# Performance work log

Hardware: AMD Instinct MI355X
Metric: run time of the kernel (lower is better)

Reference implementation:

```python
import jax, jax.numpy as jnp
import numpy as np

B, L, W, C = 16, 200, 64, 128
H_INTRA = 64   # intra_hidden // 2 per direction
H_INTER = 128
EPS = 1e-8


def layer_norm(x, gamma, beta):
    mu = jnp.mean(x, axis=-1, keepdims=True)
    var = jnp.mean(jnp.square(x - mu), axis=-1, keepdims=True)
    return (x - mu) * jax.lax.rsqrt(var + EPS) * gamma + beta


def gru_seq(x, Wk, Uk, b, H):
    """Keras GRU, reset_after=False, recurrent_activation=sigmoid. x: [N,T,D] -> [N,T,H]."""
    xw = jnp.einsum('ntd,dk->ntk', x, Wk) + b  # precompute input projections [N,T,3H]
    def step(h, xw_t):
        z = jax.nn.sigmoid(xw_t[:, :H] + h @ Uk[:, :H])
        r = jax.nn.sigmoid(xw_t[:, H:2 * H] + h @ Uk[:, H:2 * H])
        hh = jnp.tanh(xw_t[:, 2 * H:] + (r * h) @ Uk[:, 2 * H:])
        h = z * h + (1.0 - z) * hh
        return h, h
    h0 = jnp.zeros((x.shape[0], H), x.dtype)
    _, ys = jax.lax.scan(step, h0, jnp.swapaxes(xw, 0, 1))  # [T,N,H]
    return jnp.swapaxes(ys, 0, 1)


def skip_gru_seq(x, Wk, Uk, b, Wp, bp, H):
    """Skip-RNN GRU (Campos et al.): binary update gate u_t conditionally updates state.
    Returns (outputs [N,T,H], gates [N,T,1])."""
    xw = jnp.einsum('ntd,dk->ntk', x, Wk) + b
    def step(carry, xw_t):
        h, ut = carry
        # straight-through binarization of cumulative update prob
        u = ut + jax.lax.stop_gradient(jnp.round(ut) - ut)  # [N,1]
        z = jax.nn.sigmoid(xw_t[:, :H] + h @ Uk[:, :H])
        r = jax.nn.sigmoid(xw_t[:, H:2 * H] + h @ Uk[:, H:2 * H])
        hh = jnp.tanh(xw_t[:, 2 * H:] + (r * h) @ Uk[:, 2 * H:])
        h_new = z * h + (1.0 - z) * hh
        h = u * h_new + (1.0 - u) * h  # skip: copy state when u == 0
        delta = jax.nn.sigmoid(h @ Wp + bp)  # [N,1]
        ut_next = u * delta + (1.0 - u) * (ut + jnp.minimum(delta, 1.0 - ut))
        return (h, ut_next), (h, u)
    N = x.shape[0]
    h0 = jnp.zeros((N, H), x.dtype)
    ut0 = jnp.ones((N, 1), x.dtype)
    _, (ys, us) = jax.lax.scan(step, (h0, ut0), jnp.swapaxes(xw, 0, 1))
    return jnp.swapaxes(ys, 0, 1), jnp.swapaxes(us, 0, 1)


def setup_inputs():
    key = jax.random.key(0)
    ks = jax.random.split(key, 16)
    rn = lambda k, s: jax.random.normal(k, s, dtype=jnp.float32) * 0.05
    z = lambda s: jnp.zeros(s, jnp.float32)
    o = lambda s: jnp.ones(s, jnp.float32)
    return {
        'x': jax.random.normal(ks[0], (B, L, W, C), dtype=jnp.float32),
        'scale': jax.random.uniform(ks[1], (B, L, W, 1), dtype=jnp.float32),
        'Wf': rn(ks[2], (C, 3 * H_INTRA)), 'Uf': rn(ks[3], (H_INTRA, 3 * H_INTRA)), 'bf': z((3 * H_INTRA,)),
        'Wb': rn(ks[4], (C, 3 * H_INTRA)), 'Ub': rn(ks[5], (H_INTRA, 3 * H_INTRA)), 'bb': z((3 * H_INTRA,)),
        'W_intra_fc': rn(ks[6], (2 * H_INTRA, C)), 'b_intra_fc': z((C,)),
        'g_intra': o((C,)), 'beta_intra': z((C,)),
        'Wi': rn(ks[7], (C + 1, 3 * H_INTER)), 'Ui': rn(ks[8], (H_INTER, 3 * H_INTER)), 'bi': z((3 * H_INTER,)),
        'Wp': rn(ks[9], (H_INTER, 1)), 'bp': z((1,)),
        'W_inter_fc': rn(ks[10], (H_INTER, C)), 'b_inter_fc': z((C,)),
        'g_inter': o((C,)), 'beta_inter': z((C,)),
    }


def reference(x, scale, Wf, Uf, bf, Wb, Ub, bb, W_intra_fc, b_intra_fc, g_intra, beta_intra,
              Wi, Ui, bi, Wp, bp, W_inter_fc, b_inter_fc, g_inter, beta_inter):
    # ----- intra path: bidirectional GRU over the width axis -----
    intra_in = x.reshape(B * L, W, C)
    out_f = gru_seq(intra_in, Wf, Uf, bf, H_INTRA)
    out_b = gru_seq(intra_in[:, ::-1, :], Wb, Ub, bb, H_INTRA)[:, ::-1, :]
    intra_rnn_out = jnp.concatenate([out_f, out_b], axis=-1)  # [B*L, W, 2H]
    update_gate_intra = jnp.ones((64, L), jnp.float32)  # skip=0 branch: constant ones
    intra_dense = intra_rnn_out @ W_intra_fc + b_intra_fc  # [B*L, W, C]
    intra_out = x + layer_norm(intra_dense.reshape(B, L, W, C), g_intra, beta_intra)
    # ----- inter path: skip-GRU over the L (time) axis -----
    inter_in = jnp.transpose(intra_out, (0, 2, 1, 3)).reshape(B * W, L, C)
    scale2 = jnp.transpose(scale, (0, 2, 1, 3)).reshape(B * W, L, 1)
    inter_in = jnp.concatenate([inter_in, scale2], axis=-1)  # [B*W, L, C+1]
    inter_rnn_out, gates = skip_gru_seq(inter_in, Wi, Ui, bi, Wp, bp, H_INTER)
    update_gate_inter = gates[:, :, 0]  # [B*W, L]
    inter_dense = (inter_rnn_out @ W_inter_fc + b_inter_fc).reshape(B, W, L, C)
    inter_ln_in = jnp.transpose(inter_dense, (0, 2, 1, 3))  # [B, L, W, C]
    inter_out = intra_out + layer_norm(inter_ln_in, g_inter, beta_inter)
    return inter_out, update_gate_intra, update_gate_inter
```

## Files before the change

### kernel.cpp

```cpp
#include <hip/hip_runtime.h>
#include <cmath>


typedef float f32x16 __attribute__((ext_vector_type(16)));

__device__ __forceinline__ float sigf(float x) { return 1.0f / (1.0f + expf(-x)); }
__device__ __forceinline__ float rlanef(float v, int l) {
  return __uint_as_float(__builtin_amdgcn_readlane(__float_as_uint(v), (unsigned)l));
}
__device__ __forceinline__ void ldsbar() {
  asm volatile("s_waitcnt lgkmcnt(0)" ::: "memory");
  __builtin_amdgcn_s_barrier();
  __builtin_amdgcn_sched_barrier(0);
}

template <int SB>
__device__ __forceinline__ void macP2(const f32x16& u0, const f32x16& u1, float hv,
                                      float& a0, float& a1) {
#pragma unroll
  for (int k = 0; k < 16; ++k) {
    const float hs = rlanef(hv, SB + k);
    a0 = fmaf(u0[k], hs, a0);
    a1 = fmaf(u1[k], hs, a1);
  }
}
template <int SB>
__device__ __forceinline__ void macP1(const f32x16& u, float hv, float& a) {
#pragma unroll
  for (int k = 0; k < 16; ++k) a = fmaf(u[k], rlanef(hv, SB + k), a);
}

__global__ __launch_bounds__(256) void k_fill_ones(float* __restrict__ p, int n) {
  int i = blockIdx.x * 256 + threadIdx.x;
  if (i < n) p[i] = 1.0f;
}

enum { MA_X_FWD = 0, MA_X_BWD = 1, MA_INTER = 2 };

template <int MODE>
__global__ __launch_bounds__(256) void k_gemm_xw(
    const float* __restrict__ A0, const float* __restrict__ A1,
    const float* __restrict__ Bm, const float* __restrict__ bias,
    float* __restrict__ Cm, long M0, int N, int K, int KT)
{
  __shared__ float As[16][132];
  __shared__ float Bs[16][68];
  const int tid = threadIdx.x;
  const int tx = tid & 15, ty = tid >> 4;
  const long row0g = M0 + (long)blockIdx.x * 128;
  const int col0 = blockIdx.y * 64;
  const int lr = tid >> 1;
  const int lk8 = (tid & 1) * 8;
  const int bk = tid >> 4;
  const int bc4 = (tid & 15) * 4;
  float acc[8][4];
#pragma unroll
  for (int i = 0; i < 8; ++i)
#pragma unroll
    for (int j = 0; j < 4; ++j) acc[i][j] = 0.f;

  const long rg = row0g + lr;
  long abase = 0, rowc = 0;
  if (MODE == MA_X_FWD) {
    abase = rg * 128;
  } else if (MODE == MA_X_BWD) {
    const long s = rg >> 6; const int t = (int)(rg & 63);
    abase = (s * 64 + (63 - t)) * 128;
  } else {
    const int n = (int)(rg & 1023);
    const int l = (int)(rg >> 10);
    rowc = ((long)(n >> 6) * 200 + l) * 64 + (n & 63);
    abase = rowc * 128;
  }

  for (int kt = 0; kt < KT; ++kt) {
    const int k0 = kt * 16;
    {
      float v[8];
      if (MODE != MA_INTER || kt < 8) {
        const float4 a0 = *reinterpret_cast<const float4*>(&A0[abase + k0 + lk8]);
        const float4 a1 = *reinterpret_cast<const float4*>(&A0[abase + k0 + lk8 + 4]);
        v[0] = a0.x; v[1] = a0.y; v[2] = a0.z; v[3] = a0.w;
        v[4] = a1.x; v[5] = a1.y; v[6] = a1.z; v[7] = a1.w;
      } else {
#pragma unroll
        for (int j = 0; j < 8; ++j) {
          const int k = k0 + lk8 + j;
          v[j] = (k < 128) ? A0[abase + k] : ((k == 128) ? A1[rowc] : 0.f);
        }
      }
#pragma unroll
      for (int j = 0; j < 8; ++j) As[lk8 + j][lr] = v[j];
    }
    {
      const int k = k0 + bk;
      float4 b4 = make_float4(0.f, 0.f, 0.f, 0.f);
      if (k < K) b4 = *reinterpret_cast<const float4*>(&Bm[(long)k * N + col0 + bc4]);
      *reinterpret_cast<float4*>(&Bs[bk][bc4]) = b4;
    }
    __syncthreads();
#pragma unroll
    for (int kk = 0; kk < 16; ++kk) {
      const float4 a0 = *reinterpret_cast<const float4*>(&As[kk][ty * 8]);
      const float4 a1 = *reinterpret_cast<const float4*>(&As[kk][ty * 8 + 4]);
      const float4 b4 = *reinterpret_cast<const float4*>(&Bs[kk][tx * 4]);
      const float av[8] = {a0.x, a0.y, a0.z, a0.w, a1.x, a1.y, a1.z, a1.w};
      const float bv[4] = {b4.x, b4.y, b4.z, b4.w};
#pragma unroll
      for (int i = 0; i < 8; ++i)
#pragma unroll
        for (int j = 0; j < 4; ++j) acc[i][j] = fmaf(av[i], bv[j], acc[i][j]);
    }
    __syncthreads();
  }
  const float4 bi4 = *reinterpret_cast<const float4*>(&bias[col0 + tx * 4]);
#pragma unroll
  for (int i = 0; i < 8; ++i) {
    const long rl = (long)blockIdx.x * 128 + ty * 8 + i;
    float4 o;
    o.x = acc[i][0] + bi4.x;
    o.y = acc[i][1] + bi4.y;
    o.z = acc[i][2] + bi4.z;
    o.w = acc[i][3] + bi4.w;
    *reinterpret_cast<float4*>(&Cm[rl * (long)N + col0 + tx * 4]) = o;
  }
}

__global__ __attribute__((amdgpu_waves_per_eu(4, 4))) __launch_bounds__(256)
void k_gru_intra5(
    const float* __restrict__ xwf, const float* __restrict__ xwb,
    const float* __restrict__ Uf, const float* __restrict__ Ub,
    float* __restrict__ rnn)
{
  const int dir = blockIdx.y;
  const float* __restrict__ xw = dir ? xwb : xwf;
  const float* __restrict__ U  = dir ? Ub : Uf;
  __shared__ float h8[4][64], z8[4][64], rh8[4][64];
  __shared__ float pA[4][4][128];
  __shared__ float pB[4][4][64];
  const int tid = threadIdx.x;
  const int w = tid >> 6, lane = tid & 63;
  const long s0 = (long)blockIdx.x * 4;

  f32x16 uz, ur, uhh;
#pragma unroll
  for (int k = 0; k < 16; ++k) {
    const int row = (w * 16 + k) * 192;
    uz[k]  = U[row + lane];
    ur[k]  = U[row + 64 + lane];
    uhh[k] = U[row + 128 + lane];
  }
  h8[w][lane] = 0.f;
  __syncthreads();

  const long xrow0 = (s0 + w) * 64;
  float xa1 = xw[xrow0 * 192 + lane];
  float xa2 = xw[xrow0 * 192 + 64 + lane];
  float xb  = xw[xrow0 * 192 + 128 + lane];

  for (int t = 0; t < 64; ++t) {
    const int tn = (t < 63) ? t + 1 : t;
    const float xa1n = xw[(xrow0 + tn) * 192 + lane];
    const float xa2n = xw[(xrow0 + tn) * 192 + 64 + lane];
    const float xbn  = xw[(xrow0 + tn) * 192 + 128 + lane];
    {
      const float hv01 = h8[lane >> 5][w * 16 + (lane & 15)];
      const float hv23 = h8[2 + (lane >> 5)][w * 16 + (lane & 15)];
      float az0 = 0.f, ar0 = 0.f, az1 = 0.f, ar1 = 0.f;
      float az2 = 0.f, ar2 = 0.f, az3 = 0.f, ar3 = 0.f;
      macP2<0>(uz, ur, hv01, az0, ar0);
      macP2<32>(uz, ur, hv01, az1, ar1);
      macP2<0>(uz, ur, hv23, az2, ar2);
      macP2<32>(uz, ur, hv23, az3, ar3);
      pA[0][w][lane] = az0; pA[0][w][64 + lane] = ar0;
      pA[1][w][lane] = az1; pA[1][w][64 + lane] = ar1;
      pA[2][w][lane] = az2; pA[2][w][64 + lane] = ar2;
      pA[3][w][lane] = az3; pA[3][w][64 + lane] = ar3;
    }
    ldsbar();
    {
      const float sz = pA[w][0][lane] + pA[w][1][lane] + pA[w][2][lane] +
                       pA[w][3][lane] + xa1;
      const float sr = pA[w][0][64 + lane] + pA[w][1][64 + lane] +
                       pA[w][2][64 + lane] + pA[w][3][64 + lane] + xa2;
      z8[w][lane] = sigf(sz);
      rh8[w][lane] = sigf(sr) * h8[w][lane];
    }
    ldsbar();
    {
      const float rv01 = rh8[lane >> 5][w * 16 + (lane & 15)];
      const float rv23 = rh8[2 + (lane >> 5)][w * 16 + (lane & 15)];
      float a0 = 0.f, a1 = 0.f, a2 = 0.f, a3 = 0.f;
      macP1<0>(uhh, rv01, a0);
      macP1<32>(uhh, rv01, a1);
      macP1<0>(uhh, rv23, a2);
      macP1<32>(uhh, rv23, a3);
      pB[0][w][lane] = a0;
      pB[1][w][lane] = a1;
      pB[2][w][lane] = a2;
      pB[3][w][lane] = a3;
    }
    ldsbar();
    {
      const float pre = pB[w][0][lane] + pB[w][1][lane] + pB[w][2][lane] +
                        pB[w][3][lane] + xb;
      const float hh = tanhf(pre);
      const float z = z8[w][lane];
      const float ho = h8[w][lane];
      const float hn = z * ho + (1.f - z) * hh;
      h8[w][lane] = hn;
      const int tt = dir ? (63 - t) : t;
      rnn[((s0 + w) * 64 + tt) * 128 + dir * 64 + lane] = hn;
    }
    ldsbar();
    xa1 = xa1n; xa2 = xa2n; xb = xbn;
  }
}

__global__ __attribute__((amdgpu_waves_per_eu(4, 4))) __launch_bounds__(1024)
void k_gru_inter10(
    const float* __restrict__ xw, const float* __restrict__ Ui,
    const float* __restrict__ Wp, const float* __restrict__ bp,
    float* __restrict__ rnn, float* __restrict__ gates,
    float* __restrict__ hstate, float* __restrict__ ustate,
    int t0, int nt)
{
  __shared__ float h4[4][128], z4[4][128], rh4[4][128];
  __shared__ float pA[4][8][256];
  __shared__ float pB[4][8][128];
  __shared__ float uu[4], utt[4];
  const int tid = threadIdx.x;
  const int w = tid >> 6, lane = tid & 63;
  const int kq = w & 7;
  const int kb = kq << 4;
  const int cg = w >> 3;
  const int n0 = blockIdx.x * 4;

  f32x16 uz0, uz1, uh;
#pragma unroll
  for (int k = 0; k < 16; ++k) {
    const long r = (long)(kb + k) * 384;
    uz0[k] = Ui[r + cg * 128 + lane];
    uz1[k] = Ui[r + cg * 128 + 64 + lane];
    uh[k]  = Ui[r + 256 + cg * 64 + lane];
  }
  if (tid < 512) {
    const int s = tid >> 7, c = tid & 127;
    h4[s][c] = (t0 == 0) ? 0.f : hstate[(long)(n0 + s) * 128 + c];
  }
  if (tid < 4) {
    utt[tid] = (t0 == 0) ? 1.f : ustate[n0 + tid];
    uu[tid]  = (t0 == 0) ? 1.f : ustate[1024 + n0 + tid];
  }
  const float bp0 = bp[0];
  float wpA = 0.f, wpB = 0.f;
  if (w < 4) { wpA = Wp[lane]; wpB = Wp[64 + lane]; }
  __syncthreads();

  const int sC = tid >> 8;
  const int cC = tid & 255;
  float xc = xw[(long)(n0 + sC) * 384 + cC];
  float xbA = 0.f, xbB = 0.f;
  if (w < 4) {
    xbA = xw[(long)(n0 + w) * 384 + 256 + lane];
    xbB = xw[(long)(n0 + w) * 384 + 320 + lane];
  }

  for (int dl = 0; dl < nt; ++dl) {
    const float u0g = uu[0], u1g = uu[1], u2g = uu[2], u3g = uu[3];
    const bool act = (u0g + u1g + u2g + u3g) != 0.f;
    const int dn = (dl + 1 < nt) ? dl + 1 : dl;
    const float xcn = xw[((long)dn * 1024 + n0 + sC) * 384 + cC];
    float xbAn = 0.f, xbBn = 0.f;
    if (w < 4) {
      xbAn = xw[((long)dn * 1024 + n0 + w) * 384 + 256 + lane];
      xbBn = xw[((long)dn * 1024 + n0 + w) * 384 + 320 + lane];
    }
    if (act) {
      {
        const float hv01 = h4[lane >> 5][kb + (lane & 15)];
        const float hv23 = h4[2 + (lane >> 5)][kb + (lane & 15)];
        if (u0g != 0.f) {
          float a0 = 0.f, a1 = 0.f;
          macP2<0>(uz0, uz1, hv01, a0, a1);
          pA[0][kq][cg * 128 + lane] = a0;
          pA[0][kq][cg * 128 + 64 + lane] = a1;
        }
        if (u1g != 0.f) {
          float a0 = 0.f, a1 = 0.f;
          macP2<32>(uz0, uz1, hv01, a0, a1);
          pA[1][kq][cg * 128 + lane] = a0;
          pA[1][kq][cg * 128 + 64 + lane] = a1;
        }
        if (u2g != 0.f) {
          float a0 = 0.f, a1 = 0.f;
          macP2<0>(uz0, uz1, hv23, a0, a1);
          pA[2][kq][cg * 128 + lane] = a0;
          pA[2][kq][cg * 128 + 64 + lane] = a1;
        }
        if (u3g != 0.f) {
          float a0 = 0.f, a1 = 0.f;
          macP2<32>(uz0, uz1, hv23, a0, a1);
          pA[3][kq][cg * 128 + lane] = a0;
          pA[3][kq][cg * 128 + 64 + lane] = a1;
        }
      }
      ldsbar();
      {
        if (uu[sC] != 0.f) {
          float sum = xc;
#pragma unroll
          for (int q = 0; q < 8; ++q) sum += pA[sC][q][cC];
          if (cC < 128) z4[sC][cC] = sigf(sum);
          else rh4[sC][cC - 128] = sigf(sum) * h4[sC][cC - 128];
        }
      }
      ldsbar();
      {
        const float rv01 = rh4[lane >> 5][kb + (lane & 15)];
        const float rv23 = rh4[2 + (lane >> 5)][kb + (lane & 15)];
        const int cB = cg * 64 + lane;
        if (u0g != 0.f) {
          float b = 0.f;
          macP1<0>(uh, rv01, b);
          pB[0][kq][cB] = b;
        }
        if (u1g != 0.f) {
          float b = 0.f;
          macP1<32>(uh, rv01, b);
          pB[1][kq][cB] = b;
        }
        if (u2g != 0.f) {
          float b = 0.f;
          macP1<0>(uh, rv23, b);
          pB[2][kq][cB] = b;
        }
        if (u3g != 0.f) {
          float b = 0.f;
          macP1<32>(uh, rv23, b);
          pB[3][kq][cB] = b;
        }
      }
      ldsbar();
      if (w < 4) {
        const float us = uu[w];
        const float hoA = h4[w][lane], hoB = h4[w][64 + lane];
        float hqA, hqB;
        if (us != 0.f) {
          float sA = xbA, sB = xbB;
#pragma unroll
          for (int q = 0; q < 8; ++q) {
            sA += pB[w][q][lane];
            sB += pB[w][q][64 + lane];
          }
          const float hhA = tanhf(sA), hhB = tanhf(sB);
          const float zA = z4[w][lane], zB = z4[w][64 + lane];
          hqA = zA * hoA + (1.f - zA) * hhA;
          hqB = zB * hoB + (1.f - zB) * hhB;
          h4[w][lane] = hqA;
          h4[w][64 + lane] = hqB;
        } else {
          hqA = hoA; hqB = hoB;
        }
        rnn[((long)dl * 1024 + n0 + w) * 128 + lane] = hqA;
        rnn[((long)dl * 1024 + n0 + w) * 128 + 64 + lane] = hqB;
        float p = hqA * wpA + hqB * wpB;
        p += __shfl_xor(p, 32);
        p += __shfl_xor(p, 16);
        p += __shfl_xor(p, 8);
        p += __shfl_xor(p, 4);
        p += __shfl_xor(p, 2);
        p += __shfl_xor(p, 1);
        if (lane == 0) {
          const float delta = sigf(p + bp0);
          const float ut = utt[w];
          gates[(long)(n0 + w) * 200 + t0 + dl] = us;
          const float utn = us * delta + (1.f - us) * (ut + fminf(delta, 1.f - ut));
          utt[w] = utn;
          uu[w] = rintf(utn);
        }
      }
    } else {
      if (w < 4) {
        const float hqA = h4[w][lane], hqB = h4[w][64 + lane];
        rnn[((long)dl * 1024 + n0 + w) * 128 + lane] = hqA;
        rnn[((long)dl * 1024 + n0 + w) * 128 + 64 + lane] = hqB;
        float p = hqA * wpA + hqB * wpB;
        p += __shfl_xor(p, 32);
        p += __shfl_xor(p, 16);
        p += __shfl_xor(p, 8);
        p += __shfl_xor(p, 4);
        p += __shfl_xor(p, 2);
        p += __shfl_xor(p, 1);
        if (lane == 0) {
          const float delta = sigf(p + bp0);
          const float ut = utt[w];
          gates[(long)(n0 + w) * 200 + t0 + dl] = 0.f;
          const float utn = ut + fminf(delta, 1.f - ut);
          utt[w] = utn;
          uu[w] = rintf(utn);
        }
      }
    }
    ldsbar();
    xc = xcn; xbA = xbAn; xbB = xbBn;
  }
  if (tid < 512) {
    const int s = tid >> 7, c = tid & 127;
    hstate[(long)(n0 + s) * 128 + c] = h4[s][c];
  }
  if (tid < 4) {
    ustate[n0 + tid] = utt[tid];
    ustate[1024 + n0 + tid] = uu[tid];
  }
}

template <int OM>
__global__ __launch_bounds__(256) void k_fcln(
    const float* __restrict__ A, const float* __restrict__ Wt,
    const float* __restrict__ bias, const float* __restrict__ gamma,
    const float* __restrict__ beta, const float* __restrict__ resid,
    float* __restrict__ dst, long M0)
{
  __shared__ float As[16][68];
  __shared__ float Bs[16][132];
  __shared__ float red0[64][33];
  __shared__ float red1[64][33];
  __shared__ float mu_s[64];
  __shared__ float rs_s[64];
  const int tid = threadIdx.x;
  const int tx = tid & 31, ty = tid >> 5;
  const long r0l = (long)blockIdx.x * 64;
  const int lr = tid >> 2;
  const int lk4 = (tid & 3) * 4;
  const int bkk = tid >> 4;
  const int bc8 = (tid & 15) * 8;
  float acc[8][4];
#pragma unroll
  for (int i = 0; i < 8; ++i)
#pragma unroll
    for (int j = 0; j < 4; ++j) acc[i][j] = 0.f;

  for (int kt = 0; kt < 8; ++kt) {
    const int k0 = kt * 16;
    {
      const float4 a4 = *reinterpret_cast<const float4*>(&A[(r0l + lr) * 128 + k0 + lk4]);
      As[lk4 + 0][lr] = a4.x;
      As[lk4 + 1][lr] = a4.y;
      As[lk4 + 2][lr] = a4.z;
      As[lk4 + 3][lr] = a4.w;
    }
    {
      const float4 w0 = *reinterpret_cast<const float4*>(&Wt[(long)(k0 + bkk) * 128 + bc8]);
      const float4 w1 = *reinterpret_cast<const float4*>(&Wt[(long)(k0 + bkk) * 128 + bc8 + 4]);
      *reinterpret_cast<float4*>(&Bs[bkk][bc8]) = w0;
      *reinterpret_cast<float4*>(&Bs[bkk][bc8 + 4]) = w1;
    }
    __syncthreads();
#pragma unroll
    for (int kk = 0; kk < 16; ++kk) {
      const float4 a0 = *reinterpret_cast<const float4*>(&As[kk][ty * 8]);
      const float4 a1 = *reinterpret_cast<const float4*>(&As[kk][ty * 8 + 4]);
      const float4 b4 = *reinterpret_cast<const float4*>(&Bs[kk][tx * 4]);
      const float av[8] = {a0.x, a0.y, a0.z, a0.w, a1.x, a1.y, a1.z, a1.w};
      const float bv[4] = {b4.x, b4.y, b4.z, b4.w};
#pragma unroll
      for (int i = 0; i < 8; ++i)
#pragma unroll
        for (int j = 0; j < 4; ++j) acc[i][j] = fmaf(av[i], bv[j], acc[i][j]);
    }
    __syncthreads();
  }
  {
    const float4 bb4 = *reinterpret_cast<const float4*>(&bias[tx * 4]);
#pragma unroll
    for (int i = 0; i < 8; ++i) {
      acc[i][0] += bb4.x;
      acc[i][1] += bb4.y;
      acc[i][2] += bb4.z;
      acc[i][3] += bb4.w;
    }
  }
#pragma unroll
  for (int i = 0; i < 8; ++i) {
    const float s = acc[i][0] + acc[i][1] + acc[i][2] + acc[i][3];
    const float q = acc[i][0] * acc[i][0] + acc[i][1] * acc[i][1] +
                    acc[i][2] * acc[i][2] + acc[i][3] * acc[i][3];
    red0[ty * 8 + i][tx] = s;
    red1[ty * 8 + i][tx] = q;
  }
  __syncthreads();
  if (tid < 64) {
    float s = 0.f, q = 0.f;
#pragma unroll
    for (int j = 0; j < 32; ++j) { s += red0[tid][j]; q += red1[tid][j]; }
    const float mu = s * (1.0f / 128.0f);
    const float var = q * (1.0f / 128.0f) - mu * mu;
    mu_s[tid] = mu;
    rs_s[tid] = 1.0f / sqrtf(var + 1e-8f);
  }
  __syncthreads();
  const float4 g4 = *reinterpret_cast<const float4*>(&gamma[tx * 4]);
  const float4 be4 = *reinterpret_cast<const float4*>(&beta[tx * 4]);
#pragma unroll
  for (int i = 0; i < 8; ++i) {
    const int rloc = ty * 8 + i;
    const long rg = M0 + r0l + rloc;
    long off;
    if (OM == 0) {
      off = rg * 128 + tx * 4;
    } else {
      const int n = (int)(rg & 1023);
      const int l = (int)(rg >> 10);
      off = (((long)(n >> 6) * 200 + l) * 64 + (n & 63)) * 128 + tx * 4;
    }
    const float4 r4 = *reinterpret_cast<const float4*>(&resid[off]);
    const float mu = mu_s[rloc], rs = rs_s[rloc];
    float4 o;
    o.x = (acc[i][0] - mu) * rs * g4.x + be4.x + r4.x;
    o.y = (acc[i][1] - mu) * rs * g4.y + be4.y + r4.y;
    o.z = (acc[i][2] - mu) * rs * g4.z + be4.z + r4.z;
    o.w = (acc[i][3] - mu) * rs * g4.w + be4.w + r4.w;
    *reinterpret_cast<float4*>(&dst[off]) = o;
  }
}

extern "C" void kernel_launch(void* const* d_in, const int* in_sizes, int n_in,
                              void* d_out, int out_size, void* d_ws, size_t ws_size,
                              hipStream_t stream)
{
  (void)in_sizes; (void)n_in; (void)out_size;
  const float* x    = (const float*)d_in[0];
  const float* scl  = (const float*)d_in[1];
  const float* Wf   = (const float*)d_in[2];
  const float* Uf   = (const float*)d_in[3];
  const float* bf   = (const float*)d_in[4];
  const float* Wb   = (const float*)d_in[5];
  const float* Ub   = (const float*)d_in[6];
  const float* bb   = (const float*)d_in[7];
  const float* Wfc1 = (const float*)d_in[8];
  const float* bfc1 = (const float*)d_in[9];
  const float* gam1 = (const float*)d_in[10];
  const float* bet1 = (const float*)d_in[11];
  const float* Wi   = (const float*)d_in[12];
  const float* Ui   = (const float*)d_in[13];
  const float* bi   = (const float*)d_in[14];
  const float* Wp   = (const float*)d_in[15];
  const float* bp   = (const float*)d_in[16];
  const float* Wfc2 = (const float*)d_in[17];
  const float* bfc2 = (const float*)d_in[18];
  const float* gam2 = (const float*)d_in[19];
  const float* bet2 = (const float*)d_in[20];

  float* outp  = (float*)d_out;
  float* io    = outp;
  float* onesp = outp + 26214400L;
  float* gates = outp + 26214400L + 12800L;
  float* ws    = (float*)d_ws;
  const long wsf = (long)(ws_size / sizeof(float));

  k_fill_ones<<<50, 256, 0, stream>>>(onesp, 12800);

  long cnI = (wsf / 32768L) & ~7L;
  if (cnI > 3200) cnI = 3200;
  if (cnI < 8) cnI = 8;
  for (long s0 = 0; s0 < 3200; s0 += cnI) {
    const long cn = (3200 - s0 < cnI) ? (3200 - s0) : cnI;
    float* xwf = ws;
    float* xwb = ws + cn * 12288L;
    float* rnn = ws + cn * 24576L;
    const long M = cn * 64;
    dim3 gg((unsigned)(M / 128), 3);
    k_gemm_xw<MA_X_FWD><<<gg, 256, 0, stream>>>(x, nullptr, Wf, bf, xwf, s0 * 64, 192, 128, 8);
    k_gemm_xw<MA_X_BWD><<<gg, 256, 0, stream>>>(x, nullptr, Wb, bb, xwb, s0 * 64, 192, 128, 8);
    dim3 gr((unsigned)(cn / 4), 2);
    k_gru_intra5<<<gr, 256, 0, stream>>>(xwf, xwb, Uf, Ub, rnn);
    k_fcln<0><<<(unsigned)(M / 64), 256, 0, stream>>>(rnn, Wfc1, bfc1, gam1, bet1, x, io, s0 * 64);
  }

  const long per_t = 1024L * 384 + 1024L * 128;
  const long state_f = 1024L * 128 + 3072L;
  long nt_alloc = (wsf - state_f) / per_t;
  if (nt_alloc > 200) nt_alloc = 200;
  if (nt_alloc < 1) nt_alloc = 1;
  float* xwi    = ws;
  float* rnnI   = ws + nt_alloc * 1024L * 384;
  float* hstate = rnnI + nt_alloc * 1024L * 128;
  float* ustate = hstate + 1024L * 128;

  for (long t0 = 0; t0 < 200; t0 += nt_alloc) {
    const int nt = (int)((200 - t0 < nt_alloc) ? (200 - t0) : nt_alloc);
    dim3 gg((unsigned)(8 * nt), 6);
    k_gemm_xw<MA_INTER><<<gg, 256, 0, stream>>>(io, scl, Wi, bi, xwi, t0 * 1024, 384, 129, 9);
    k_gru_inter10<<<256, 1024, 0, stream>>>(xwi, Ui, Wp, bp, rnnI, gates, hstate, ustate,
                                            (int)t0, nt);
    k_fcln<1><<<(unsigned)(16 * nt), 256, 0, stream>>>(rnnI, Wfc2, bfc2, gam2, bet2, io, outp,
                                                       t0 * 1024);
  }
}
```

Measured before the change: 1.808 ms.

## Specialize inter GRU waves into z/r and candidate groups

Restructures the inter skip-GRU kernel so waves 0-7 each own a 16-row K slice of the z/r recurrent weights (64 registers) and waves 8-15 own the candidate weights. This replaces the earlier uniform split where every wave held pieces of all three gates. The skip-all branch is merged into the common path, and the custom LDS barriers become __syncthreads. The goal is fewer redundant lane broadcasts per FMA and a more even split of recurrent work. The cost is idle waves during each phase and higher register pressure for the z/r waves.

```diff
diff --git a/kernel.cpp b/kernel.cpp
--- a/kernel.cpp
+++ b/kernel.cpp
@@ -15,17 +15,30 @@
 }
 
 template <int SB>
-__device__ __forceinline__ void macP2(const f32x16& u0, const f32x16& u1, float hv,
-                                      float& a0, float& a1) {
+__device__ __forceinline__ void mac4(const f32x16& u0, const f32x16& u1,
+                                     const f32x16& u2, const f32x16& u3, float hv,
+                                     float& a0, float& a1, float& a2, float& a3) {
 #pragma unroll
   for (int k = 0; k < 16; ++k) {
     const float hs = rlanef(hv, SB + k);
     a0 = fmaf(u0[k], hs, a0);
     a1 = fmaf(u1[k], hs, a1);
+    a2 = fmaf(u2[k], hs, a2);
+    a3 = fmaf(u3[k], hs, a3);
   }
 }
 template <int SB>
-__device__ __forceinline__ void macP1(const f32x16& u, float hv, float& a) {
+__device__ __forceinline__ void mac2(const f32x16& u0, const f32x16& u1, float hv,
+                                     float& a0, float& a1) {
+#pragma unroll
+  for (int k = 0; k < 16; ++k) {
+    const float hs = rlanef(hv, SB + k);
+    a0 = fmaf(u0[k], hs, a0);
+    a1 = fmaf(u1[k], hs, a1);
+  }
+}
+template <int SB>
+__device__ __forceinline__ void mac1(const f32x16& u, float hv, float& a) {
 #pragma unroll
   for (int k = 0; k < 16; ++k) a = fmaf(u[k], rlanef(hv, SB + k), a);
 }
@@ -168,10 +181,10 @@
       const float hv23 = h8[2 + (lane >> 5)][w * 16 + (lane & 15)];
       float az0 = 0.f, ar0 = 0.f, az1 = 0.f, ar1 = 0.f;
       float az2 = 0.f, ar2 = 0.f, az3 = 0.f, ar3 = 0.f;
-      macP2<0>(uz, ur, hv01, az0, ar0);
-      macP2<32>(uz, ur, hv01, az1, ar1);
-      macP2<0>(uz, ur, hv23, az2, ar2);
-      macP2<32>(uz, ur, hv23, az3, ar3);
+      mac2<0>(uz, ur, hv01, az0, ar0);
+      mac2<32>(uz, ur, hv01, az1, ar1);
+      mac2<0>(uz, ur, hv23, az2, ar2);
+      mac2<32>(uz, ur, hv23, az3, ar3);
       pA[0][w][lane] = az0; pA[0][w][64 + lane] = ar0;
       pA[1][w][lane] = az1; pA[1][w][64 + lane] = ar1;
       pA[2][w][lane] = az2; pA[2][w][64 + lane] = ar2;
@@ -191,10 +204,10 @@
       const float rv01 = rh8[lane >> 5][w * 16 + (lane & 15)];
       const float rv23 = rh8[2 + (lane >> 5)][w * 16 + (lane & 15)];
       float a0 = 0.f, a1 = 0.f, a2 = 0.f, a3 = 0.f;
-      macP1<0>(uhh, rv01, a0);
-      macP1<32>(uhh, rv01, a1);
-      macP1<0>(uhh, rv23, a2);
-      macP1<32>(uhh, rv23, a3);
+      mac1<0>(uhh, rv01, a0);
+      mac1<32>(uhh, rv01, a1);
+      mac1<0>(uhh, rv23, a2);
+      mac1<32>(uhh, rv23, a3);
       pB[0][w][lane] = a0;
       pB[1][w][lane] = a1;
       pB[2][w][lane] = a2;
@@ -217,8 +230,7 @@
   }
 }
 
-__global__ __attribute__((amdgpu_waves_per_eu(4, 4))) __launch_bounds__(1024)
-void k_gru_inter10(
+__global__ __launch_bounds__(1024, 4) void k_gru_inter4(
     const float* __restrict__ xw, const float* __restrict__ Ui,
     const float* __restrict__ Wp, const float* __restrict__ bp,
     float* __restrict__ rnn, float* __restrict__ gates,
@@ -231,18 +243,27 @@
   __shared__ float uu[4], utt[4];
   const int tid = threadIdx.x;
   const int w = tid >> 6, lane = tid & 63;
-  const int kq = w & 7;
-  const int kb = kq << 4;
-  const int cg = w >> 3;
   const int n0 = blockIdx.x * 4;
-
-  f32x16 uz0, uz1, uh;
-#pragma unroll
-  for (int k = 0; k < 16; ++k) {
-    const long r = (long)(kb + k) * 384;
-    uz0[k] = Ui[r + cg * 128 + lane];
-    uz1[k] = Ui[r + cg * 128 + 64 + lane];
-    uh[k]  = Ui[r + 256 + cg * 64 + lane];
+  const bool isZR = (w < 8);
+
+  f32x16 uA0, uA1, uA2, uA3;
+  if (isZR) {
+#pragma unroll
+    for (int k = 0; k < 16; ++k) {
+      const long r = (long)(w * 16 + k) * 384;
+      uA0[k] = Ui[r + lane];
+      uA1[k] = Ui[r + 64 + lane];
+      uA2[k] = Ui[r + 128 + lane];
+      uA3[k] = Ui[r + 192 + lane];
+    }
+  } else {
+    const int ks = w - 8;
+#pragma unroll
+    for (int k = 0; k < 16; ++k) {
+      const long r = (long)(ks * 16 + k) * 384 + 256;
+      uA0[k] = Ui[r + lane];
+      uA1[k] = Ui[r + 64 + lane];
+    }
   }
   if (tid < 512) {
     const int s = tid >> 7, c = tid & 127;
@@ -253,13 +274,13 @@
     uu[tid]  = (t0 == 0) ? 1.f : ustate[1024 + n0 + tid];
   }
   const float bp0 = bp[0];
-  float wpA = 0.f, wpB = 0.f;
-  if (w < 4) { wpA = Wp[lane]; wpB = Wp[64 + lane]; }
+  float wprA = 0.f, wprB = 0.f;
+  if (w < 4) { wprA = Wp[lane]; wprB = Wp[64 + lane]; }
   __syncthreads();
 
-  const int sC = tid >> 8;
-  const int cC = tid & 255;
-  float xc = xw[(long)(n0 + sC) * 384 + cC];
+  const int cs = w >> 2;
+  const int cc = (w & 3) * 64 + lane;
+  float xc = xw[(long)(n0 + cs) * 384 + cc];
   float xbA = 0.f, xbB = 0.f;
   if (w < 4) {
     xbA = xw[(long)(n0 + w) * 384 + 256 + lane];
@@ -270,139 +291,116 @@
     const float u0g = uu[0], u1g = uu[1], u2g = uu[2], u3g = uu[3];
     const bool act = (u0g + u1g + u2g + u3g) != 0.f;
     const int dn = (dl + 1 < nt) ? dl + 1 : dl;
-    const float xcn = xw[((long)dn * 1024 + n0 + sC) * 384 + cC];
+    const float xcn = xw[((long)dn * 1024 + n0 + cs) * 384 + cc];
     float xbAn = 0.f, xbBn = 0.f;
     if (w < 4) {
       xbAn = xw[((long)dn * 1024 + n0 + w) * 384 + 256 + lane];
       xbBn = xw[((long)dn * 1024 + n0 + w) * 384 + 320 + lane];
     }
     if (act) {
+      if (isZR) {
+        const float hv = h4[lane >> 4][w * 16 + (lane & 15)];
+        if (u0g != 0.f) {
+          float a0 = 0.f, a1 = 0.f, a2 = 0.f, a3 = 0.f;
+          mac4<0>(uA0, uA1, uA2, uA3, hv, a0, a1, a2, a3);
+          pA[0][w][lane] = a0; pA[0][w][64 + lane] = a1;
+          pA[0][w][128 + lane] = a2; pA[0][w][192 + lane] = a3;
+        }
+        if (u1g != 0.f) {
+          float a0 = 0.f, a1 = 0.f, a2 = 0.f, a3 = 0.f;
+          mac4<16>(uA0, uA1, uA2, uA3, hv, a0, a1, a2, a3);
+          pA[1][w][lane] = a0; pA[1][w][64 + lane] = a1;
+          pA[1][w][128 + lane] = a2; pA[1][w][192 + lane] = a3;
+        }
+        if (u2g != 0.f) {
+          float a0 = 0.f, a1 = 0.f, a2 = 0.f, a3 = 0.f;
+          mac4<32>(uA0, uA1, uA2, uA3, hv, a0, a1, a2, a3);
+          pA[2][w][lane] = a0; pA[2][w][64 + lane] = a1;
+          pA[2][w][128 + lane] = a2; pA[2][w][192 + lane] = a3;
+        }
+        if (u3g != 0.f) {
+          float a0 = 0.f, a1 = 0.f, a2 = 0.f, a3 = 0.f;
+          mac4<48>(uA0, uA1, uA2, uA3, hv, a0, a1, a2, a3);
+          pA[3][w][lane] = a0; pA[3][w][64 + lane] = a1;
+          pA[3][w][128 + lane] = a2; pA[3][w][192 + lane] = a3;
+        }
+      }
+      __syncthreads();
       {
-        const float hv01 = h4[lane >> 5][kb + (lane & 15)];
-        const float hv23 = h4[2 + (lane >> 5)][kb + (lane & 15)];
+        if (uu[cs] != 0.f) {
+          float sum = xc;
+#pragma unroll
+          for (int ks = 0; ks < 8; ++ks) sum += pA[cs][ks][cc];
+          if (cc < 128) z4[cs][cc] = sigf(sum);
+          else rh4[cs][cc - 128] = sigf(sum) * h4[cs][cc - 128];
+        }
+      }
+      __syncthreads();
+      if (!isZR) {
+        const int ks = w - 8;
+        const float rv = rh4[lane >> 4][ks * 16 + (lane & 15)];
         if (u0g != 0.f) {
-          float a0 = 0.f, a1 = 0.f;
-          macP2<0>(uz0, uz1, hv01, a0, a1);
-          pA[0][kq][cg * 128 + lane] = a0;
-          pA[0][kq][cg * 128 + 64 + lane] = a1;
+          float b0 = 0.f, b1 = 0.f;
+          mac2<0>(uA0, uA1, rv, b0, b1);
+          pB[0][ks][lane] = b0; pB[0][ks][64 + lane] = b1;
         }
         if (u1g != 0.f) {
-          float a0 = 0.f, a1 = 0.f;
-          macP2<32>(uz0, uz1, hv01, a0, a1);
-          pA[1][kq][cg * 128 + lane] = a0;
-          pA[1][kq][cg * 128 + 64 + lane] = a1;
+          float b0 = 0.f, b1 = 0.f;
+          mac2<16>(uA0, uA1, rv, b0, b1);
+          pB[1][ks][lane] = b0; pB[1][ks][64 + lane] = b1;
         }
         if (u2g != 0.f) {
-          float a0 = 0.f, a1 = 0.f;
-          macP2<0>(uz0, uz1, hv23, a0, a1);
-          pA[2][kq][cg * 128 + lane] = a0;
-          pA[2][kq][cg * 128 + 64 + lane] = a1;
+          float b0 = 0.f, b1 = 0.f;
+          mac2<32>(uA0, uA1, rv, b0, b1);
+          pB[2][ks][lane] = b0; pB[2][ks][64 + lane] = b1;
         }
         if (u3g != 0.f) {
-          float a0 = 0.f, a1 = 0.f;
-          macP2<32>(uz0, uz1, hv23, a0, a1);
-          pA[3][kq][cg * 128 + lane] = a0;
-          pA[3][kq][cg * 128 + 64 + lane] = a1;
+          float b0 = 0.f, b1 = 0.f;
+          mac2<48>(uA0, uA1, rv, b0, b1);
+          pB[3][ks][lane] = b0; pB[3][ks][64 + lane] = b1;
         }
       }
-      ldsbar();
-      {
-        if (uu[sC] != 0.f) {
-          float sum = xc;
-#pragma unroll
-          for (int q = 0; q < 8; ++q) sum += pA[sC][q][cC];
-          if (cC < 128) z4[sC][cC] = sigf(sum);
-          else rh4[sC][cC - 128] = sigf(sum) * h4[sC][cC - 128];
-        }
+      __syncthreads();
+    }
+    if (w < 4) {
+      const float us = uu[w];
+      const float hoA = h4[w][lane], hoB = h4[w][64 + lane];
+      float hqA, hqB;
+      if (us != 0.f) {
+        float sA = xbA, sB = xbB;
+#pragma unroll
+        for (int ks = 0; ks < 8; ++ks) {
+          sA += pB[w][ks][lane];
+          sB += pB[w][ks][64 + lane];
+        }
+        const float hhA = tanhf(sA), hhB = tanhf(sB);
+        const float zA = z4[w][lane], zB = z4[w][64 + lane];
+        hqA = zA * hoA + (1.f - zA) * hhA;
+        hqB = zB * hoB + (1.f - zB) * hhB;
+        h4[w][lane] = hqA;
+        h4[w][64 + lane] = hqB;
+      } else {
+        hqA = hoA; hqB = hoB;
       }
-      ldsbar();
-      {
-        const float rv01 = rh4[lane >> 5][kb + (lane & 15)];
-        const float rv23 = rh4[2 + (lane >> 5)][kb + (lane & 15)];
-        const int cB = cg * 64 + lane;
-        if (u0g != 0.f) {
-          float b = 0.f;
-          macP1<0>(uh, rv01, b);
-          pB[0][kq][cB] = b;
-        }
-        if (u1g != 0.f) {
-          float b = 0.f;
-          macP1<32>(uh, rv01, b);
-          pB[1][kq][cB] = b;
-        }
-        if (u2g != 0.f) {
-          float b = 0.f;
-          macP1<0>(uh, rv23, b);
-          pB[2][kq][cB] = b;
-        }
-        if (u3g != 0.f) {
-          float b = 0.f;
-          macP1<32>(uh, rv23, b);
-          pB[3][kq][cB] = b;
-        }
+      rnn[((long)dl * 1024 + n0 + w) * 128 + lane] = hqA;
+      rnn[((long)dl * 1024 + n0 + w) * 128 + 64 + lane] = hqB;
+      float p = hqA * wprA + hqB * wprB;
+      p += __shfl_xor(p, 32);
+      p += __shfl_xor(p, 16);
+      p += __shfl_xor(p, 8);
+      p += __shfl_xor(p, 4);
+      p += __shfl_xor(p, 2);
+      p += __shfl_xor(p, 1);
+      const float delta = sigf(p + bp0);
+      const float ut = utt[w];
+      const float utn = us * delta + (1.f - us) * (ut + fminf(delta, 1.f - ut));
+      if (lane == 0) {
+        gates[(long)(n0 + w) * 200 + t0 + dl] = us;
+        utt[w] = utn;
+        uu[w] = rintf(utn);
       }
-      ldsbar();
-      if (w < 4) {
-        const float us = uu[w];
-        const float hoA = h4[w][lane], hoB = h4[w][64 + lane];
-        float hqA, hqB;
-        if (us != 0.f) {
-          float sA = xbA, sB = xbB;
-#pragma unroll
-          for (int q = 0; q < 8; ++q) {
-            sA += pB[w][q][lane];
-            sB += pB[w][q][64 + lane];
-          }
-          const float hhA = tanhf(sA), hhB = tanhf(sB);
-          const float zA = z4[w][lane], zB = z4[w][64 + lane];
-          hqA = zA * hoA + (1.f - zA) * hhA;
-          hqB = zB * hoB + (1.f - zB) * hhB;
-          h4[w][lane] = hqA;
-          h4[w][64 + lane] = hqB;
-        } else {
-          hqA = hoA; hqB = hoB;
-        }
-        rnn[((long)dl * 1024 + n0 + w) * 128 + lane] = hqA;
-        rnn[((long)dl * 1024 + n0 + w) * 128 + 64 + lane] = hqB;
-        float p = hqA * wpA + hqB * wpB;
-        p += __shfl_xor(p, 32);
-        p += __shfl_xor(p, 16);
-        p += __shfl_xor(p, 8);
-        p += __shfl_xor(p, 4);
-        p += __shfl_xor(p, 2);
-        p += __shfl_xor(p, 1);
-        if (lane == 0) {
-          const float delta = sigf(p + bp0);
-          const float ut = utt[w];
-          gates[(long)(n0 + w) * 200 + t0 + dl] = us;
-          const float utn = us * delta + (1.f - us) * (ut + fminf(delta, 1.f - ut));
-          utt[w] = utn;
-          uu[w] = rintf(utn);
-        }
-      }
-    } else {
-      if (w < 4) {
-        const float hqA = h4[w][lane], hqB = h4[w][64 + lane];
-        rnn[((long)dl * 1024 + n0 + w) * 128 + lane] = hqA;
-        rnn[((long)dl * 1024 + n0 + w) * 128 + 64 + lane] = hqB;
-        float p = hqA * wpA + hqB * wpB;
-        p += __shfl_xor(p, 32);
-        p += __shfl_xor(p, 16);
-        p += __shfl_xor(p, 8);
-        p += __shfl_xor(p, 4);
-        p += __shfl_xor(p, 2);
-        p += __shfl_xor(p, 1);
-        if (lane == 0) {
-          const float delta = sigf(p + bp0);
-          const float ut = utt[w];
-          gates[(long)(n0 + w) * 200 + t0 + dl] = 0.f;
-          const float utn = ut + fminf(delta, 1.f - ut);
-          utt[w] = utn;
-          uu[w] = rintf(utn);
-        }
-      }
-    }
-    ldsbar();
+    }
+    __syncthreads();
     xc = xcn; xbA = xbAn; xbB = xbBn;
   }
   if (tid < 512) {
@@ -592,8 +590,8 @@
     const int nt = (int)((200 - t0 < nt_alloc) ? (200 - t0) : nt_alloc);
     dim3 gg((unsigned)(8 * nt), 6);
     k_gemm_xw<MA_INTER><<<gg, 256, 0, stream>>>(io, scl, Wi, bi, xwi, t0 * 1024, 384, 129, 9);
-    k_gru_inter10<<<256, 1024, 0, stream>>>(xwi, Ui, Wp, bp, rnnI, gates, hstate, ustate,
-                                            (int)t0, nt);
+    k_gru_inter4<<<256, 1024, 0, stream>>>(xwi, Ui, Wp, bp, rnnI, gates, hstate, ustate,
+                                           (int)t0, nt);
     k_fcln<1><<<(unsigned)(16 * nt), 256, 0, stream>>>(rnnI, Wfc2, bfc2, gam2, bet2, io, outp,
                                                        t0 * 1024);
   }
```

Measured after the change: 1.760 ms. -2.6%, faster.
